# Performance work log

Hardware: AMD Instinct MI355X
Metric: run time of the kernel (lower is better)

Reference implementation:

```python
import jax, jax.numpy as jnp
import numpy as np

B, N, FIN, FOUT = 64, 784, 64, 64
EPS = 1e-5
NEG = -1e9  # masked-logit fill (avoids -inf NaNs on isolated nodes)


def setup_inputs() -> dict:
    key = jax.random.key(0)
    ks = jax.random.split(key, 6)
    init = lambda k, shape, fan: (jax.random.normal(k, shape, jnp.float32) / np.float32(np.sqrt(fan)))
    return {
        "node_features": jax.random.normal(ks[0], (B, N, FIN), jnp.float32),
        "adjacency_matrix": jax.random.randint(ks[1], (N, N), 0, 2, jnp.int32),
        "W_self": init(ks[2], (FOUT, FIN), FIN),
        "b_self": jnp.zeros((FOUT,), jnp.float32),
        "W_nb": init(ks[3], (FOUT, FIN), FIN),
        "b_nb": jnp.zeros((FOUT,), jnp.float32),
        "a_src": init(ks[4], (FIN,), 2 * FIN),   # attention weight half acting on x_i
        "a_dst": init(ks[5], (FIN,), 2 * FIN),   # attention weight half acting on x_j
        "b_att": jnp.zeros((), jnp.float32),
        "ln_gamma": jnp.ones((FOUT,), jnp.float32),
        "ln_beta": jnp.zeros((FOUT,), jnp.float32),
    }


def reference(node_features, adjacency_matrix, W_self, b_self, W_nb, b_nb,
              a_src, a_dst, b_att, ln_gamma, ln_beta):
    # mask[i, j] = node j is a neighbor of node i
    mask = adjacency_matrix != 0  # [N, N]

    self_feats = node_features @ W_self.T + b_self      # [B, N, Fout]
    nb_proj = node_features @ W_nb.T + b_nb              # [B, N, Fout]

    # attention(cat[x_i, x_j]) == x_i @ a_src + x_j @ a_dst + b_att
    src = node_features @ a_src                          # [B, N]
    dst = node_features @ a_dst                          # [B, N]
    logits = src[:, :, None] + dst[:, None, :] + b_att   # [B, N, N]
    logits = jnp.where(mask[None], logits, NEG)
    # softmax over neighbors j; zero out non-edges (handles isolated nodes -> 0)
    w = jax.nn.softmax(logits, axis=2) * mask[None]
    agg = jnp.einsum('bij,bjf->bif', w, nb_proj)         # [B, N, Fout]

    combined = self_feats + agg                           # dropout: eval mode (identity)
    mu = combined.mean(-1, keepdims=True)
    var = combined.var(-1, keepdims=True)
    normed = (combined - mu) * jax.lax.rsqrt(var + EPS) * ln_gamma + ln_beta
    return jax.nn.relu(normed)
```

## Files before the change

kernel.cpp:

```cpp
#include <hip/hip_runtime.h>


typedef unsigned short u16;
typedef unsigned int u32;
typedef short bf16x8 __attribute__((ext_vector_type(8)));
typedef float f32x4 __attribute__((ext_vector_type(4)));

#define NNODE 784
#define MP 832
#define BUFU 13312

__device__ __forceinline__ float b2f(u16 h) {
  union { u32 u; float f; } v; v.u = ((u32)h) << 16; return v.f;
}
__device__ __forceinline__ u16 f2b(float f) {
  union { float f; u32 u; } v; v.f = f;
  u32 r = (v.u + 0x7FFFu + ((v.u >> 16) & 1u)) >> 16;
  return (u16)r;
}
__device__ __forceinline__ void gload16(const u16* g, u16* l) {
  __builtin_amdgcn_global_load_lds((const __attribute__((address_space(1))) u32*)g,
                                   (__attribute__((address_space(3))) u32*)l, 16, 0, 0);
}

__global__ __launch_bounds__(256) void k_pre(const int* __restrict__ adj,
                                             const float* __restrict__ Ws,
                                             const float* __restrict__ Wn,
                                             const float* __restrict__ X,
                                             const float* __restrict__ adst,
                                             u16* __restrict__ A,
                                             u16* __restrict__ W2,
                                             u16* __restrict__ Bt) {
  const int bid = blockIdx.x;
  const int t = threadIdx.x;
  if (bid < 364) {
    int idx8 = bid * 256 + t;
    int i = idx8 / 104, j8 = idx8 - i * 104;
    __align__(16) u16 o[8];
    if (i < NNODE && j8 < 98) {
      const int4* ap = (const int4*)(adj + (size_t)i * NNODE + j8 * 8);
      int4 a0 = ap[0], a1 = ap[1];
      o[0] = a0.x ? 0x3F80 : 0; o[1] = a0.y ? 0x3F80 : 0;
      o[2] = a0.z ? 0x3F80 : 0; o[3] = a0.w ? 0x3F80 : 0;
      o[4] = a1.x ? 0x3F80 : 0; o[5] = a1.y ? 0x3F80 : 0;
      o[6] = a1.z ? 0x3F80 : 0; o[7] = a1.w ? 0x3F80 : 0;
    } else {
#pragma unroll
      for (int q = 0; q < 8; ++q) o[q] = 0;
    }
    *(uint4*)(A + (size_t)i * MP + j8 * 8) = *(const uint4*)o;
    return;
  }
  if (bid == 364) {
    int f = t >> 2, cq = t & 3;
#pragma unroll
    for (int q = 0; q < 4; ++q) {
      int c = cq * 4 + q;
      int cs = c ^ (f & 7);
      const float* src = (cs < 8) ? (Ws + f * 64 + cs * 8) : (Wn + f * 64 + (cs - 8) * 8);
      float4 v0 = ((const float4*)src)[0], v1 = ((const float4*)src)[1];
      __align__(16) u16 ob[8];
      ob[0] = f2b(v0.x); ob[1] = f2b(v0.y); ob[2] = f2b(v0.z); ob[3] = f2b(v0.w);
      ob[4] = f2b(v1.x); ob[5] = f2b(v1.y); ob[6] = f2b(v1.z); ob[7] = f2b(v1.w);
      *(uint4*)(W2 + f * 128 + c * 8) = *(const uint4*)ob;
    }
    return;
  }
  __shared__ float Xs[64][68];
  __shared__ float ad[64];
  __shared__ float es[64];
  int bid2 = bid - 365;
  int b = bid2 / 13, jt = bid2 - b * 13;
  int j0 = jt * 64;
  if (b == 64) {
    int row = 4160 + (t >> 2), c = (t & 3) * 16;
    uint4 z; z.x = 0; z.y = 0; z.z = 0; z.w = 0;
    uint4* p = (uint4*)(Bt + (size_t)row * MP + j0 + c);
    p[0] = z; p[1] = z;
    return;
  }
  int jr = t >> 2, cg = t & 3;
  {
    int j = j0 + jr;
    float4 z4; z4.x = 0.f; z4.y = 0.f; z4.z = 0.f; z4.w = 0.f;
    float4 v0 = z4, v1 = z4, v2 = z4, v3 = z4;
    if (j < NNODE) {
      const float4* xp = (const float4*)(X + ((size_t)b * NNODE + j) * 64 + cg * 16);
      v0 = xp[0]; v1 = xp[1]; v2 = xp[2]; v3 = xp[3];
    }
    float4* d = (float4*)&Xs[jr][cg * 16];
    d[0] = v0; d[1] = v1; d[2] = v2; d[3] = v3;
  }
  if (t < 64) ad[t] = adst[t];
  __syncthreads();
  {
    float dot = 0.f;
#pragma unroll
    for (int q = 0; q < 16; ++q) dot += Xs[jr][cg * 16 + q] * ad[cg * 16 + q];
    dot += __shfl_xor(dot, 1);
    dot += __shfl_xor(dot, 2);
    if (cg == 0) es[jr] = (j0 + jr < NNODE) ? __expf(dot) : 0.f;
  }
  __syncthreads();
  {
    int f = t >> 2, jc = (t & 3) * 16;
    __align__(16) u16 ob[16];
#pragma unroll
    for (int q = 0; q < 16; ++q) ob[q] = f2b(es[jc + q] * Xs[jc + q][f]);
    u16* op = Bt + ((size_t)b * 64 + f) * MP + j0 + jc;
    *(uint4*)op = *(const uint4*)ob;
    *(uint4*)(op + 8) = *(const uint4*)(ob + 8);
  }
  if (t < 64) Bt[(size_t)(4096 + b) * MP + j0 + t] = f2b(es[t]);
}

__global__ __launch_bounds__(512, 4) void k_gt(const u16* __restrict__ A,
                                               const u16* __restrict__ Bt,
                                               const u16* __restrict__ W2g,
                                               const float* __restrict__ X,
                                               const float* __restrict__ bs,
                                               const float* __restrict__ bn,
                                               const float* __restrict__ gam,
                                               const float* __restrict__ bet,
                                               float* __restrict__ out) {
  __shared__ __align__(16) u16 lds[2 * BUFU];
  __shared__ float denL[64][2];
  __shared__ float bsL[64], bnL[64], gamL[64], betL[64];
  const int t = threadIdx.x;
  const int l = t & 63, w = t >> 6;
  const int g = l >> 4, l15 = l & 15;
  const int wr = w >> 2, wc = w & 3;

  int wg = (blockIdx.x & 7) * 52 + (blockIdx.x >> 3);
  const int bp = wg / 13;
  const int it = wg - bp * 13;
  const int i0 = it * 64;
  const int nb0 = bp * 128;
  const int nd0 = 4096 + 2 * bp;

  if (t < 64) { bsL[t] = bs[t]; bnL[t] = bn[t]; gamL[t] = gam[t]; betL[t] = bet[t]; }

  f32x4 acc[2][2];
#pragma unroll
  for (int mi = 0; mi < 2; ++mi)
#pragma unroll
    for (int ni = 0; ni < 2; ++ni) acc[mi][ni] = (f32x4){0.f, 0.f, 0.f, 0.f};
  f32x4 accD[2];
  accD[0] = (f32x4){0.f, 0.f, 0.f, 0.f};
  accD[1] = (f32x4){0.f, 0.f, 0.f, 0.f};

#define STAGE(kt_, buf_)                                                          \
  {                                                                               \
    int k0_ = (kt_) * 64;                                                         \
    u16* dA_ = lds + (buf_) * BUFU;                                               \
    u16* dB_ = dA_ + 4096;                                                        \
    { int r_ = t >> 3, c_ = t & 7;                                                \
      gload16(A + (size_t)(i0 + r_) * MP + k0_ + ((c_ ^ (r_ & 7)) * 8),           \
              dA_ + w * 512); }                                                   \
    _Pragma("unroll")                                                             \
    for (int h_ = 0; h_ < 2; ++h_) {                                              \
      int s_ = h_ * 512 + t; int r_ = s_ >> 3, c_ = s_ & 7;                       \
      gload16(Bt + (size_t)(nb0 + r_) * MP + k0_ + ((c_ ^ (r_ & 7)) * 8),         \
              dB_ + h_ * 4096 + w * 512); }                                       \
    if (w < 2) { int r_ = t >> 3, c_ = t & 7;                                     \
      gload16(Bt + (size_t)(nd0 + r_) * MP + k0_ + ((c_ ^ (r_ & 7)) * 8),         \
              dB_ + 8192 + w * 512); }                                            \
  }

  STAGE(0, 0);
  __syncthreads();

  for (int kt = 0; kt < 13; ++kt) {
    int buf = kt & 1;
    if (kt < 12) STAGE(kt + 1, buf ^ 1);
    const u16* As = lds + buf * BUFU;
    const u16* Bs = As + 4096;
#pragma unroll
    for (int kk = 0; kk < 2; ++kk) {
      int q = kk * 4 + g;
      bf16x8 af[2], bfr[2];
#pragma unroll
      for (int mi = 0; mi < 2; ++mi) {
        int ra = wr * 32 + mi * 16 + l15;
        af[mi] = *(const bf16x8*)(As + ra * 64 + ((q ^ (ra & 7)) * 8));
      }
#pragma unroll
      for (int ni = 0; ni < 2; ++ni) {
        int rb = wc * 32 + ni * 16 + l15;
        bfr[ni] = *(const bf16x8*)(Bs + rb * 64 + ((q ^ (rb & 7)) * 8));
      }
#pragma unroll
      for (int mi = 0; mi < 2; ++mi)
#pragma unroll
        for (int ni = 0; ni < 2; ++ni)
          acc[mi][ni] = __builtin_amdgcn_mfma_f32_16x16x32_bf16(af[mi], bfr[ni], acc[mi][ni], 0, 0, 0);
      if (wc == 2 + kk) {
        int rd = 128 + l15;
        bf16x8 bd = *(const bf16x8*)(Bs + rd * 64 + ((q ^ (rd & 7)) * 8));
        accD[0] = __builtin_amdgcn_mfma_f32_16x16x32_bf16(af[0], bd, accD[0], 0, 0, 0);
        accD[1] = __builtin_amdgcn_mfma_f32_16x16x32_bf16(af[1], bd, accD[1], 0, 0, 0);
      }
    }
    __syncthreads();
  }
#undef STAGE

  u16* AB2 = lds;
  u16* W2l = lds + 16384;
  if (wc == 2 && l15 < 2) {
#pragma unroll
    for (int mi = 0; mi < 2; ++mi)
#pragma unroll
      for (int j = 0; j < 4; ++j)
        denL[wr * 32 + mi * 16 + g * 4 + j][l15] = accD[mi][j];
  }
#pragma unroll
  for (int q2 = 0; q2 < 2; ++q2) {
    int s = q2 * 512 + t;
    int r = s >> 3, c = s & 7;
    int i = i0 + (r & 63);
    int bq = bp * 2 + (r >> 6);
    float4 v0, v1;
    v0.x = v0.y = v0.z = v0.w = 0.f; v1 = v0;
    if (i < NNODE) {
      const float4* xp = (const float4*)(X + ((size_t)bq * NNODE + i) * 64 + c * 8);
      v0 = xp[0]; v1 = xp[1];
    }
    __align__(16) u16 ob[8];
    ob[0] = f2b(v0.x); ob[1] = f2b(v0.y); ob[2] = f2b(v0.z); ob[3] = f2b(v0.w);
    ob[4] = f2b(v1.x); ob[5] = f2b(v1.y); ob[6] = f2b(v1.z); ob[7] = f2b(v1.w);
    *(uint4*)(AB2 + r * 128 + ((c ^ (r & 7)) * 8)) = *(const uint4*)ob;
  }
#pragma unroll
  for (int q2 = 0; q2 < 2; ++q2)
    gload16(W2g + q2 * 4096 + w * 512 + l * 8, W2l + q2 * 4096 + w * 512);
  __syncthreads();

  if (wc == 3 && l15 < 2) {
#pragma unroll
    for (int mi = 0; mi < 2; ++mi)
#pragma unroll
      for (int j = 0; j < 4; ++j)
        denL[wr * 32 + mi * 16 + g * 4 + j][l15] += accD[mi][j];
  }
  __syncthreads();

#pragma unroll
  for (int mi = 0; mi < 2; ++mi)
#pragma unroll
    for (int ni = 0; ni < 2; ++ni) {
      int col = wc * 32 + ni * 16 + l15;
      int b2 = col >> 6, f = col & 63;
#pragma unroll
      for (int j = 0; j < 4; ++j) {
        int ri = wr * 32 + mi * 16 + g * 4 + j;
        float d = denL[ri][b2];
        float rd = d > 0.f ? 1.f / d : 0.f;
        int R = b2 * 64 + ri;
        AB2[R * 128 + (((8 + (f >> 3)) ^ (R & 7)) * 8) + (f & 7)] = f2b(acc[mi][ni][j] * rd);
      }
    }
  __syncthreads();

  const int b2w = w >> 2, mf = w & 3;
  f32x4 a2[4];
#pragma unroll
  for (int nf = 0; nf < 4; ++nf) a2[nf] = (f32x4){0.f, 0.f, 0.f, 0.f};
#pragma unroll
  for (int kk = 0; kk < 4; ++kk) {
    int q2 = kk * 4 + g;
    int ra = b2w * 64 + mf * 16 + l15;
    bf16x8 af = *(const bf16x8*)(AB2 + ra * 128 + ((q2 ^ (ra & 7)) * 8));
#pragma unroll
    for (int nf = 0; nf < 4; ++nf) {
      int rb = nf * 16 + l15;
      bf16x8 bfw = *(const bf16x8*)(W2l + rb * 128 + ((q2 ^ (rb & 7)) * 8));
      a2[nf] = __builtin_amdgcn_mfma_f32_16x16x32_bf16(af, bfw, a2[nf], 0, 0, 0);
    }
  }

#pragma unroll
  for (int j = 0; j < 4; ++j) {
    int ri = mf * 16 + g * 4 + j;
    float d = denL[ri][b2w];
    float bnm = d > 0.f ? 1.f : 0.f;
    float v0 = a2[0][j] + bsL[l15]      + bnm * bnL[l15];
    float v1 = a2[1][j] + bsL[l15 + 16] + bnm * bnL[l15 + 16];
    float v2 = a2[2][j] + bsL[l15 + 32] + bnm * bnL[l15 + 32];
    float v3 = a2[3][j] + bsL[l15 + 48] + bnm * bnL[l15 + 48];
    float s1 = v0 + v1 + v2 + v3;
    float s2 = v0 * v0 + v1 * v1 + v2 * v2 + v3 * v3;
    s1 += __shfl_xor(s1, 1); s2 += __shfl_xor(s2, 1);
    s1 += __shfl_xor(s1, 2); s2 += __shfl_xor(s2, 2);
    s1 += __shfl_xor(s1, 4); s2 += __shfl_xor(s2, 4);
    s1 += __shfl_xor(s1, 8); s2 += __shfl_xor(s2, 8);
    float mu = s1 * (1.f / 64.f);
    float var = fmaxf(s2 * (1.f / 64.f) - mu * mu, 0.f);
    float inv = rsqrtf(var + 1e-5f);
    int node = i0 + ri;
    if (node < NNODE) {
      float* op = out + ((size_t)(bp * 2 + b2w) * NNODE + node) * 64;
      op[l15]      = fmaxf((v0 - mu) * inv * gamL[l15]      + betL[l15],      0.f);
      op[l15 + 16] = fmaxf((v1 - mu) * inv * gamL[l15 + 16] + betL[l15 + 16], 0.f);
      op[l15 + 32] = fmaxf((v2 - mu) * inv * gamL[l15 + 32] + betL[l15 + 32], 0.f);
      op[l15 + 48] = fmaxf((v3 - mu) * inv * gamL[l15 + 48] + betL[l15 + 48], 0.f);
    }
  }
}

extern "C" void kernel_launch(void* const* d_in, const int* in_sizes, int n_in,
                              void* d_out, int out_size, void* d_ws, size_t ws_size,
                              hipStream_t stream) {
  const float* X     = (const float*)d_in[0];
  const int*   adj   = (const int*)d_in[1];
  const float* Wself = (const float*)d_in[2];
  const float* bself = (const float*)d_in[3];
  const float* Wnb   = (const float*)d_in[4];
  const float* bnb   = (const float*)d_in[5];
  const float* adst  = (const float*)d_in[7];
  const float* gam   = (const float*)d_in[9];
  const float* bet   = (const float*)d_in[10];
  float* out = (float*)d_out;
  char* ws = (char*)d_ws;

  u16* Apad = (u16*)(ws);
  u16* W2g  = (u16*)(ws + 1490944);
  u16* Bt   = (u16*)(ws + 1507328);

  k_pre<<<dim3(1210), dim3(256), 0, stream>>>(adj, Wself, Wnb, X, adst, Apad, W2g, Bt);
  k_gt <<<dim3(416),  dim3(512), 0, stream>>>(Apad, Bt, W2g, X, bself, bnb, gam, bet, out);
}
```

Baseline: 30.20 us.

## Fuse preprocessing and GEMM kernels into one persistent kernel with grid barrier

```diff
diff --git a/kernel.cpp b/kernel.cpp
--- a/kernel.cpp
+++ b/kernel.cpp
@@ -23,122 +23,25 @@
                                    (__attribute__((address_space(3))) u32*)l, 16, 0, 0);
 }
 
-__global__ __launch_bounds__(256) void k_pre(const int* __restrict__ adj,
-                                             const float* __restrict__ Ws,
-                                             const float* __restrict__ Wn,
-                                             const float* __restrict__ X,
-                                             const float* __restrict__ adst,
-                                             u16* __restrict__ A,
-                                             u16* __restrict__ W2,
-                                             u16* __restrict__ Bt) {
-  const int bid = blockIdx.x;
-  const int t = threadIdx.x;
-  if (bid < 364) {
-    int idx8 = bid * 256 + t;
-    int i = idx8 / 104, j8 = idx8 - i * 104;
-    __align__(16) u16 o[8];
-    if (i < NNODE && j8 < 98) {
-      const int4* ap = (const int4*)(adj + (size_t)i * NNODE + j8 * 8);
-      int4 a0 = ap[0], a1 = ap[1];
-      o[0] = a0.x ? 0x3F80 : 0; o[1] = a0.y ? 0x3F80 : 0;
-      o[2] = a0.z ? 0x3F80 : 0; o[3] = a0.w ? 0x3F80 : 0;
-      o[4] = a1.x ? 0x3F80 : 0; o[5] = a1.y ? 0x3F80 : 0;
-      o[6] = a1.z ? 0x3F80 : 0; o[7] = a1.w ? 0x3F80 : 0;
-    } else {
-#pragma unroll
-      for (int q = 0; q < 8; ++q) o[q] = 0;
-    }
-    *(uint4*)(A + (size_t)i * MP + j8 * 8) = *(const uint4*)o;
-    return;
-  }
-  if (bid == 364) {
-    int f = t >> 2, cq = t & 3;
-#pragma unroll
-    for (int q = 0; q < 4; ++q) {
-      int c = cq * 4 + q;
-      int cs = c ^ (f & 7);
-      const float* src = (cs < 8) ? (Ws + f * 64 + cs * 8) : (Wn + f * 64 + (cs - 8) * 8);
-      float4 v0 = ((const float4*)src)[0], v1 = ((const float4*)src)[1];
-      __align__(16) u16 ob[8];
-      ob[0] = f2b(v0.x); ob[1] = f2b(v0.y); ob[2] = f2b(v0.z); ob[3] = f2b(v0.w);
-      ob[4] = f2b(v1.x); ob[5] = f2b(v1.y); ob[6] = f2b(v1.z); ob[7] = f2b(v1.w);
-      *(uint4*)(W2 + f * 128 + c * 8) = *(const uint4*)ob;
-    }
-    return;
-  }
-  __shared__ float Xs[64][68];
-  __shared__ float ad[64];
-  __shared__ float es[64];
-  int bid2 = bid - 365;
-  int b = bid2 / 13, jt = bid2 - b * 13;
-  int j0 = jt * 64;
-  if (b == 64) {
-    int row = 4160 + (t >> 2), c = (t & 3) * 16;
-    uint4 z; z.x = 0; z.y = 0; z.z = 0; z.w = 0;
-    uint4* p = (uint4*)(Bt + (size_t)row * MP + j0 + c);
-    p[0] = z; p[1] = z;
-    return;
-  }
-  int jr = t >> 2, cg = t & 3;
-  {
-    int j = j0 + jr;
-    float4 z4; z4.x = 0.f; z4.y = 0.f; z4.z = 0.f; z4.w = 0.f;
-    float4 v0 = z4, v1 = z4, v2 = z4, v3 = z4;
-    if (j < NNODE) {
-      const float4* xp = (const float4*)(X + ((size_t)b * NNODE + j) * 64 + cg * 16);
-      v0 = xp[0]; v1 = xp[1]; v2 = xp[2]; v3 = xp[3];
-    }
-    float4* d = (float4*)&Xs[jr][cg * 16];
-    d[0] = v0; d[1] = v1; d[2] = v2; d[3] = v3;
-  }
-  if (t < 64) ad[t] = adst[t];
-  __syncthreads();
-  {
-    float dot = 0.f;
-#pragma unroll
-    for (int q = 0; q < 16; ++q) dot += Xs[jr][cg * 16 + q] * ad[cg * 16 + q];
-    dot += __shfl_xor(dot, 1);
-    dot += __shfl_xor(dot, 2);
-    if (cg == 0) es[jr] = (j0 + jr < NNODE) ? __expf(dot) : 0.f;
-  }
-  __syncthreads();
-  {
-    int f = t >> 2, jc = (t & 3) * 16;
-    __align__(16) u16 ob[16];
-#pragma unroll
-    for (int q = 0; q < 16; ++q) ob[q] = f2b(es[jc + q] * Xs[jc + q][f]);
-    u16* op = Bt + ((size_t)b * 64 + f) * MP + j0 + jc;
-    *(uint4*)op = *(const uint4*)ob;
-    *(uint4*)(op + 8) = *(const uint4*)(ob + 8);
-  }
-  if (t < 64) Bt[(size_t)(4096 + b) * MP + j0 + t] = f2b(es[t]);
-}
-
-__global__ __launch_bounds__(512, 4) void k_gt(const u16* __restrict__ A,
-                                               const u16* __restrict__ Bt,
-                                               const u16* __restrict__ W2g,
-                                               const float* __restrict__ X,
-                                               const float* __restrict__ bs,
-                                               const float* __restrict__ bn,
-                                               const float* __restrict__ gam,
-                                               const float* __restrict__ bet,
-                                               float* __restrict__ out) {
-  __shared__ __align__(16) u16 lds[2 * BUFU];
-  __shared__ float denL[64][2];
-  __shared__ float bsL[64], bnL[64], gamL[64], betL[64];
-  const int t = threadIdx.x;
+
+__device__ __forceinline__ void phaseB(const u16* __restrict__ A,
+                                       const u16* __restrict__ Bt,
+                                       const u16* __restrict__ W2g,
+                                       const float* __restrict__ X,
+                                       float* __restrict__ out,
+                                       u16* lds, float (*denL)[2],
+                                       float* bsL, float* bnL, float* gamL, float* betL,
+                                       int bid, int t) {
   const int l = t & 63, w = t >> 6;
   const int g = l >> 4, l15 = l & 15;
   const int wr = w >> 2, wc = w & 3;
 
-  int wg = (blockIdx.x & 7) * 52 + (blockIdx.x >> 3);
+  int wg = (bid & 7) * 52 + (bid >> 3);
   const int bp = wg / 13;
   const int it = wg - bp * 13;
   const int i0 = it * 64;
   const int nb0 = bp * 128;
   const int nd0 = 4096 + 2 * bp;
-
-  if (t < 64) { bsL[t] = bs[t]; bnL[t] = bn[t]; gamL[t] = gam[t]; betL[t] = bet[t]; }
 
   f32x4 acc[2][2];
 #pragma unroll
@@ -308,6 +211,234 @@
   }
 }
 
+
+__global__ __launch_bounds__(256) void k_pre(const int* __restrict__ adj,
+                                             const float* __restrict__ Ws,
+                                             const float* __restrict__ Wn,
+                                             const float* __restrict__ X,
+                                             const float* __restrict__ adst,
+                                             u16* __restrict__ A,
+                                             u16* __restrict__ W2,
+                                             u16* __restrict__ Bt) {
+  const int bid = blockIdx.x;
+  const int t = threadIdx.x;
+  if (bid < 364) {
+    int idx8 = bid * 256 + t;
+    int i = idx8 / 104, j8 = idx8 - i * 104;
+    __align__(16) u16 o[8];
+    if (i < NNODE && j8 < 98) {
+      const int4* ap = (const int4*)(adj + (size_t)i * NNODE + j8 * 8);
+      int4 a0 = ap[0], a1 = ap[1];
+      o[0] = a0.x ? 0x3F80 : 0; o[1] = a0.y ? 0x3F80 : 0;
+      o[2] = a0.z ? 0x3F80 : 0; o[3] = a0.w ? 0x3F80 : 0;
+      o[4] = a1.x ? 0x3F80 : 0; o[5] = a1.y ? 0x3F80 : 0;
+      o[6] = a1.z ? 0x3F80 : 0; o[7] = a1.w ? 0x3F80 : 0;
+    } else {
+#pragma unroll
+      for (int q = 0; q < 8; ++q) o[q] = 0;
+    }
+    *(uint4*)(A + (size_t)i * MP + j8 * 8) = *(const uint4*)o;
+    return;
+  }
+  if (bid == 364) {
+    int f = t >> 2, cq = t & 3;
+#pragma unroll
+    for (int q = 0; q < 4; ++q) {
+      int c = cq * 4 + q;
+      int cs = c ^ (f & 7);
+      const float* src = (cs < 8) ? (Ws + f * 64 + cs * 8) : (Wn + f * 64 + (cs - 8) * 8);
+      float4 v0 = ((const float4*)src)[0], v1 = ((const float4*)src)[1];
+      __align__(16) u16 ob[8];
+      ob[0] = f2b(v0.x); ob[1] = f2b(v0.y); ob[2] = f2b(v0.z); ob[3] = f2b(v0.w);
+      ob[4] = f2b(v1.x); ob[5] = f2b(v1.y); ob[6] = f2b(v1.z); ob[7] = f2b(v1.w);
+      *(uint4*)(W2 + f * 128 + c * 8) = *(const uint4*)ob;
+    }
+    return;
+  }
+  __shared__ float Xs[64][68];
+  __shared__ float ad[64];
+  __shared__ float es[64];
+  int bid2 = bid - 365;
+  int b = bid2 / 13, jt = bid2 - b * 13;
+  int j0 = jt * 64;
+  if (b == 64) {
+    int row = 4160 + (t >> 2), c = (t & 3) * 16;
+    uint4 z; z.x = 0; z.y = 0; z.z = 0; z.w = 0;
+    uint4* p = (uint4*)(Bt + (size_t)row * MP + j0 + c);
+    p[0] = z; p[1] = z;
+    return;
+  }
+  int jr = t >> 2, cg = t & 3;
+  {
+    int j = j0 + jr;
+    float4 z4; z4.x = 0.f; z4.y = 0.f; z4.z = 0.f; z4.w = 0.f;
+    float4 v0 = z4, v1 = z4, v2 = z4, v3 = z4;
+    if (j < NNODE) {
+      const float4* xp = (const float4*)(X + ((size_t)b * NNODE + j) * 64 + cg * 16);
+      v0 = xp[0]; v1 = xp[1]; v2 = xp[2]; v3 = xp[3];
+    }
+    float4* d = (float4*)&Xs[jr][cg * 16];
+    d[0] = v0; d[1] = v1; d[2] = v2; d[3] = v3;
+  }
+  if (t < 64) ad[t] = adst[t];
+  __syncthreads();
+  {
+    float dot = 0.f;
+#pragma unroll
+    for (int q = 0; q < 16; ++q) dot += Xs[jr][cg * 16 + q] * ad[cg * 16 + q];
+    dot += __shfl_xor(dot, 1);
+    dot += __shfl_xor(dot, 2);
+    if (cg == 0) es[jr] = (j0 + jr < NNODE) ? __expf(dot) : 0.f;
+  }
+  __syncthreads();
+  {
+    int f = t >> 2, jc = (t & 3) * 16;
+    __align__(16) u16 ob[16];
+#pragma unroll
+    for (int q = 0; q < 16; ++q) ob[q] = f2b(es[jc + q] * Xs[jc + q][f]);
+    u16* op = Bt + ((size_t)b * 64 + f) * MP + j0 + jc;
+    *(uint4*)op = *(const uint4*)ob;
+    *(uint4*)(op + 8) = *(const uint4*)(ob + 8);
+  }
+  if (t < 64) Bt[(size_t)(4096 + b) * MP + j0 + t] = f2b(es[t]);
+}
+
+__global__ __launch_bounds__(512, 4) void k_gt(const u16* __restrict__ A,
+                                               const u16* __restrict__ Bt,
+                                               const u16* __restrict__ W2g,
+                                               const float* __restrict__ X,
+                                               const float* __restrict__ bs,
+                                               const float* __restrict__ bn,
+                                               const float* __restrict__ gam,
+                                               const float* __restrict__ bet,
+                                               float* __restrict__ out) {
+  __shared__ __align__(16) u16 lds[2 * BUFU];
+  __shared__ float denL[64][2];
+  __shared__ float bsL[64], bnL[64], gamL[64], betL[64];
+  const int t = threadIdx.x;
+  if (t < 64) { bsL[t] = bs[t]; bnL[t] = bn[t]; gamL[t] = gam[t]; betL[t] = bet[t]; }
+  phaseB(A, Bt, W2g, X, out, lds, denL, bsL, bnL, gamL, betL, blockIdx.x, t);
+}
+
+
+__global__ __launch_bounds__(512, 4) void k_all(const int* __restrict__ adj,
+                                                const float* __restrict__ Ws,
+                                                const float* __restrict__ Wn,
+                                                const float* __restrict__ X,
+                                                const float* __restrict__ adst,
+                                                const float* __restrict__ bs,
+                                                const float* __restrict__ bn,
+                                                const float* __restrict__ gam,
+                                                const float* __restrict__ bet,
+                                                u16* __restrict__ A,
+                                                u16* __restrict__ W2g,
+                                                u16* __restrict__ Bt,
+                                                float* __restrict__ out,
+                                                u32* __restrict__ cnt) {
+  __shared__ __align__(16) u16 lds[2 * BUFU];
+  __shared__ float denL[64][2];
+  __shared__ float bsL[64], bnL[64], gamL[64], betL[64];
+  const int bid = blockIdx.x;
+  const int t = threadIdx.x;
+
+  {
+    int gtid = bid * 512 + t;
+    if (gtid < 93184) {
+      int i = gtid / 104, j8 = gtid - i * 104;
+      __align__(16) u16 o[8];
+      if (i < NNODE && j8 < 98) {
+        const int4* ap = (const int4*)(adj + (size_t)i * NNODE + j8 * 8);
+        int4 a0 = ap[0], a1 = ap[1];
+        o[0] = a0.x ? 0x3F80 : 0; o[1] = a0.y ? 0x3F80 : 0;
+        o[2] = a0.z ? 0x3F80 : 0; o[3] = a0.w ? 0x3F80 : 0;
+        o[4] = a1.x ? 0x3F80 : 0; o[5] = a1.y ? 0x3F80 : 0;
+        o[6] = a1.z ? 0x3F80 : 0; o[7] = a1.w ? 0x3F80 : 0;
+      } else {
+#pragma unroll
+        for (int q = 0; q < 8; ++q) o[q] = 0;
+      }
+      *(uint4*)(A + (size_t)i * MP + j8 * 8) = *(const uint4*)o;
+    }
+    if (bid == 415 && t < 256) {
+      int f = t >> 2, cq = t & 3;
+#pragma unroll
+      for (int q = 0; q < 4; ++q) {
+        int c = cq * 4 + q;
+        int cs = c ^ (f & 7);
+        const float* src = (cs < 8) ? (Ws + f * 64 + cs * 8) : (Wn + f * 64 + (cs - 8) * 8);
+        float4 v0 = ((const float4*)src)[0], v1 = ((const float4*)src)[1];
+        __align__(16) u16 ob[8];
+        ob[0] = f2b(v0.x); ob[1] = f2b(v0.y); ob[2] = f2b(v0.z); ob[3] = f2b(v0.w);
+        ob[4] = f2b(v1.x); ob[5] = f2b(v1.y); ob[6] = f2b(v1.z); ob[7] = f2b(v1.w);
+        *(uint4*)(W2g + f * 128 + c * 8) = *(const uint4*)ob;
+      }
+    }
+    const int sub = t >> 8, t256 = t & 255;
+    float* Xs = (float*)((char*)lds + sub * 17920);
+    float* ad = Xs + 64 * 68;
+    float* es = ad + 64;
+    const int jr = t256 >> 2, cg = t256 & 3;
+    for (int base = 0; base < 845; base += 832) {
+      int task = base + bid * 2 + sub;
+      bool valid = task < 845;
+      int b = valid ? task / 13 : 0;
+      int jt = valid ? task - b * 13 : 0;
+      int j0 = jt * 64;
+      if (valid && b == 64) {
+        int row = 4160 + (t256 >> 2), c = (t256 & 3) * 16;
+        uint4 z; z.x = 0; z.y = 0; z.z = 0; z.w = 0;
+        uint4* p = (uint4*)(Bt + (size_t)row * MP + j0 + c);
+        p[0] = z; p[1] = z;
+      }
+      bool work = valid && b < 64;
+      if (work) {
+        int j = j0 + jr;
+        float4 z4; z4.x = 0.f; z4.y = 0.f; z4.z = 0.f; z4.w = 0.f;
+        float4 v0 = z4, v1 = z4, v2 = z4, v3 = z4;
+        if (j < NNODE) {
+          const float4* xp = (const float4*)(X + ((size_t)b * NNODE + j) * 64 + cg * 16);
+          v0 = xp[0]; v1 = xp[1]; v2 = xp[2]; v3 = xp[3];
+        }
+        float4* d = (float4*)&Xs[jr * 68 + cg * 16];
+        d[0] = v0; d[1] = v1; d[2] = v2; d[3] = v3;
+        if (t256 < 64) ad[t256] = adst[t256];
+      }
+      __syncthreads();
+      if (work) {
+        float dot = 0.f;
+#pragma unroll
+        for (int q = 0; q < 16; ++q) dot += Xs[jr * 68 + cg * 16 + q] * ad[cg * 16 + q];
+        dot += __shfl_xor(dot, 1);
+        dot += __shfl_xor(dot, 2);
+        if (cg == 0) es[jr] = (j0 + jr < NNODE) ? __expf(dot) : 0.f;
+      }
+      __syncthreads();
+      if (work) {
+        int f = t256 >> 2, jc = (t256 & 3) * 16;
+        __align__(16) u16 ob[16];
+#pragma unroll
+        for (int q = 0; q < 16; ++q) ob[q] = f2b(es[jc + q] * Xs[(jc + q) * 68 + f]);
+        u16* op = Bt + ((size_t)b * 64 + f) * MP + j0 + jc;
+        *(uint4*)op = *(const uint4*)ob;
+        *(uint4*)(op + 8) = *(const uint4*)(ob + 8);
+        if (t256 < 64) Bt[(size_t)(4096 + b) * MP + j0 + t256] = f2b(es[t256]);
+      }
+      __syncthreads();
+    }
+  }
+
+  __threadfence();
+  __syncthreads();
+  if (t == 0) {
+    atomicAdd(cnt, 1u);
+    while (atomicAdd(cnt, 0u) < 416u) { __builtin_amdgcn_s_sleep(2); }
+  }
+  __syncthreads();
+
+  if (t < 64) { bsL[t] = bs[t]; bnL[t] = bn[t]; gamL[t] = gam[t]; betL[t] = bet[t]; }
+  phaseB(A, Bt, W2g, X, out, lds, denL, bsL, bnL, gamL, betL, bid, t);
+}
+
 extern "C" void kernel_launch(void* const* d_in, const int* in_sizes, int n_in,
                               void* d_out, int out_size, void* d_ws, size_t ws_size,
                               hipStream_t stream) {
@@ -326,7 +457,18 @@
   u16* Apad = (u16*)(ws);
   u16* W2g  = (u16*)(ws + 1490944);
   u16* Bt   = (u16*)(ws + 1507328);
-
-  k_pre<<<dim3(1210), dim3(256), 0, stream>>>(adj, Wself, Wnb, X, adst, Apad, W2g, Bt);
-  k_gt <<<dim3(416),  dim3(512), 0, stream>>>(Apad, Bt, W2g, X, bself, bnb, gam, bet, out);
-}
+  u32* cnt  = (u32*)(ws + 8536064);
+
+  int maxb = 0;
+  (void)hipOccupancyMaxActiveBlocksPerMultiprocessor(&maxb, k_all, 512, 0);
+
+  if (maxb >= 2) {
+    hipMemsetAsync(cnt, 0, 4, stream);
+    k_all<<<dim3(416), dim3(512), 0, stream>>>(adj, Wself, Wnb, X, adst,
+                                               bself, bnb, gam, bet,
+                                               Apad, W2g, Bt, out, cnt);
+  } else {
+    k_pre<<<dim3(1210), dim3(256), 0, stream>>>(adj, Wself, Wnb, X, adst, Apad, W2g, Bt);
+    k_gt <<<dim3(416),  dim3(512), 0, stream>>>(Apad, Bt, W2g, X, bself, bnb, gam, bet, out);
+  }
+}
```

New measurement: 30.15 us. No clear change (-0.2%).
